# Optimization experiments

Measured on AMD Instinct MI355X. Metric: run time of the kernel, lower is better.

The kernel has to match this reference:

```python
import jax, jax.numpy as jnp
import numpy as np

# irreps multiplicities: node = NSx0e + NVx1o, edge = ESx0e + EVx1o, hidden = HSx0e + HVx1o
NS, NV = 64, 32
ES, EV = 8, 8
HS, HV = 96, 32          # Gate splits HS scalars -> (HS-HV) silu scalars + HV sigmoid gates
N_NODES, N_EDGES = 10000, 100000
INV_SQRT3 = float(1.0 / np.sqrt(3.0))  # w3j(1,1,0) coefficient


def _split(x, ns, nv):
    # [N, ns + 3*nv] -> scalars [N, ns], vectors [N, nv, 3]
    return x[:, :ns], x[:, ns:].reshape(x.shape[0], nv, 3)


def _merge(s, v):
    return jnp.concatenate([s, v.reshape(v.shape[0], -1)], axis=-1)


def _fc_tp(xs, xv, ys, yv, w_ss, w_vv, w_sv, w_vs):
    """FullyConnectedTensorProduct for l<=1 irreps with path ('element') normalization.
    Paths: 0e*0e->0e, 1o*1o->0e (dot/sqrt3), 0e*1o->1o, 1o*0e->1o."""
    fan_s = w_ss.shape[0] * w_ss.shape[1] + w_vv.shape[0] * w_vv.shape[1]
    fan_v = w_sv.shape[0] * w_sv.shape[1] + w_vs.shape[0] * w_vs.shape[1]
    out_s = (jnp.einsum('eu,ev,uvw->ew', xs, ys, w_ss)
             + INV_SQRT3 * jnp.einsum('eum,evm,uvw->ew', xv, yv, w_vv)) / np.sqrt(fan_s)
    out_v = (jnp.einsum('eu,evm,uvw->ewm', xs, yv, w_sv)
             + jnp.einsum('eum,ev,uvw->ewm', xv, ys, w_vs)) / np.sqrt(fan_v)
    return out_s, out_v


def _gate(s, v, n_plain):
    # e3nn Gate: silu on plain scalars, sigmoid gates multiply each vector channel
    plain = jax.nn.silu(s[:, :n_plain])
    gates = jax.nn.sigmoid(s[:, n_plain:])
    return plain, v * gates[:, :, None]


def _lin(s, v, Ws, Wv):
    # e3nn equivariant Linear: mixes multiplicities per irrep, shared over m, 1/sqrt(fan_in)
    return (s @ Ws) / np.sqrt(Ws.shape[0]), jnp.einsum('num,uw->nwm', v, Wv) / np.sqrt(Wv.shape[0])


def setup_inputs() -> dict:
    key = jax.random.key(0)
    ks = jax.random.split(key, 15)
    rn = lambda k, sh: jax.random.normal(k, sh, dtype=jnp.float32)
    return {
        'node_features': rn(ks[0], (N_NODES, NS + 3 * NV)),
        'edge_attr': rn(ks[1], (N_EDGES, ES + 3 * EV)),
        'w_msg_ss': rn(ks[2], (NS, ES, HS)),
        'w_msg_vv': rn(ks[3], (NV, EV, HS)),
        'w_msg_sv': rn(ks[4], (NS, EV, HV)),
        'w_msg_vs': rn(ks[5], (NV, ES, HV)),
        'w_lin_msg_s': rn(ks[6], (HS - HV, HS)),
        'w_lin_msg_v': rn(ks[7], (HV, HV)),
        'w_upd_ss': rn(ks[8], (NS, HS, HS)),
        'w_upd_vv': rn(ks[9], (NV, HV, HS)),
        'w_upd_sv': rn(ks[10], (NS, HV, HV)),
        'w_upd_vs': rn(ks[11], (NV, HS, HV)),
        'w_lin_upd_s': rn(ks[12], (HS - HV, NS)),
        'w_lin_upd_v': rn(ks[13], (HV, NV)),
        'edge_index': jax.random.randint(ks[14], (2, N_EDGES), 0, N_NODES),
    }


def reference(node_features, edge_attr, w_msg_ss, w_msg_vv, w_msg_sv, w_msg_vs,
              w_lin_msg_s, w_lin_msg_v, w_upd_ss, w_upd_vv, w_upd_sv, w_upd_vs,
              w_lin_upd_s, w_lin_upd_v, edge_index):
    row, col = edge_index[0], edge_index[1]
    ns, nv = _split(node_features, NS, NV)
    es, ev = _split(edge_attr, ES, EV)

    # messages: gather -> CG tensor product -> gate -> linear
    ms, mv = _fc_tp(ns[col], nv[col], es, ev, w_msg_ss, w_msg_vv, w_msg_sv, w_msg_vs)
    ps, pv = _gate(ms, mv, HS - HV)                  # [E, HS-HV], [E, HV, 3]
    ls, lv = _lin(ps, pv, w_lin_msg_s, w_lin_msg_v)  # [E, HS],    [E, HV, 3]

    # scatter-sum aggregation onto destination nodes
    agg_s = jax.ops.segment_sum(ls, row, num_segments=N_NODES)
    agg_v = jax.ops.segment_sum(lv, row, num_segments=N_NODES)

    # node update: CG tensor product with aggregated messages -> gate -> linear -> residual
    us, uv = _fc_tp(ns, nv, agg_s, agg_v, w_upd_ss, w_upd_vv, w_upd_sv, w_upd_vs)
    gs, gv = _gate(us, uv, HS - HV)
    ds, dv = _lin(gs, gv, w_lin_upd_s, w_lin_upd_v)  # [N, NS], [N, NV, 3]
    return _merge(ns + ds, nv + dv)
```

## Files before the change

kernel.cpp:

```cpp
#include <hip/hip_runtime.h>
#include <hip/hip_bf16.h>

constexpr int kNodes = 10000;
constexpr int kEdges = 100000;

constexpr float INV_SQRT3    = 0.57735026918962576f;
constexpr float INV_SQRT768  = 0.036084391824351615f;
constexpr float INV_SQRT7168 = 0.011811389781538352f;
constexpr float INV_SQRT5120 = 0.013975424859373686f;
constexpr float INV_SQRT32   = 0.17677669529663687f;

constexpr size_t MSGW_OFF  = 0;
constexpr size_t UPDW1_OFF = 245760;
constexpr size_t UPDW2_OFF = 2080768;
constexpr size_t MLIN_OFF  = 2572288;
constexpr size_t ULIN_OFF  = 2588672;

typedef __attribute__((ext_vector_type(8))) short bf8;
typedef __attribute__((ext_vector_type(4))) float f4;
union BF { bf8 v; short s[8]; unsigned u[4]; };

__device__ __forceinline__ short f2bf(float f) {
    union { float f; unsigned u; } c; c.f = f;
    unsigned r = c.u + 0x7fffu + ((c.u >> 16) & 1u);
    return (short)(r >> 16);
}
__device__ __forceinline__ unsigned pk2(float lo, float hi) {
    union { __hip_bfloat162 h; unsigned u; } c;
    c.h = __float22bfloat162_rn(make_float2(lo, hi));
    return c.u;
}
__device__ __forceinline__ f4 mfma16(bf8 a, bf8 b, f4 c) {
    return __builtin_amdgcn_mfma_f32_16x16x32_bf16(a, b, c, 0, 0, 0);
}
__device__ __forceinline__ void gl2lds(const void* g, void* l) {
    __builtin_amdgcn_global_load_lds(
        (const __attribute__((address_space(1))) unsigned int*)g,
        (__attribute__((address_space(3))) unsigned int*)l, 16, 0, 0);
}
__device__ __forceinline__ float fsig(float x) { return 1.0f / (1.0f + __expf(-x)); }

__global__ void prep_kernel(
    const float* __restrict__ Wmss, const float* __restrict__ Wmvv,
    const float* __restrict__ Wmsv, const float* __restrict__ Wmvs,
    const float* __restrict__ Wlms, const float* __restrict__ Wlmv,
    const float* __restrict__ Wuss, const float* __restrict__ Wuvv,
    const float* __restrict__ Wusv, const float* __restrict__ Wuvs,
    const float* __restrict__ Wlus, const float* __restrict__ Wluv,
    char* __restrict__ wout)
{
    int i = blockIdx.x * 256 + threadIdx.x;
    float v = 0.f;
    short* dst;
    if (i < 122880) {
        dst = (short*)(wout + MSGW_OFF) + i;
        int t = i / 5120, q = i % 5120, r = q / 40, c = q % 40;
        if (c < 32) {
            int k = t * 32 + c;
            if (r < 96) {
                v = (k < 512 ? Wmss[k * 96 + r]
                             : Wmvv[(k - 512) * 96 + r] * INV_SQRT3) * INV_SQRT768;
            } else {
                int n2 = r - 96;
                if (k < 512) { int u = k & 63, vv = k >> 6; v = Wmsv[(u * 8 + vv) * 32 + n2] * INV_SQRT768; }
                else         { v = Wmvs[(k - 512) * 32 + n2] * INV_SQRT768; }
            }
        }
    } else if (i < 1040384) {
        int j = i - 122880;
        dst = (short*)(wout + UPDW1_OFF) + j;
        int t = j / 4096, q = j % 4096, r = q / 40, c = q % 40;
        if (q < 3840 && c < 32) {
            int k = t * 32 + c;
            if (k < 6144) { int u = k & 63, vv = k >> 6;
                v = Wuss[(u * 96 + vv) * 96 + r] * INV_SQRT7168; }
            else { int r2 = k - 6144; int u = r2 & 31, vv = r2 >> 5;
                v = Wuvv[(u * 32 + vv) * 96 + r] * (INV_SQRT3 * INV_SQRT7168); }
        }
    } else if (i < 1286144) {
        int j = i - 1040384;
        dst = (short*)(wout + UPDW2_OFF) + j;
        int t = j / 1536, q = j % 1536, r = q / 40, c = q % 40;
        if (q < 1280 && c < 32) {
            int k = t * 32 + c;
            if (k < 2048) { int u = k & 63, vv = k >> 6;
                v = Wusv[(u * 32 + vv) * 32 + r] * INV_SQRT5120; }
            else { int r2 = k - 2048;
                v = Wuvs[r2 * 32 + r] * INV_SQRT5120; }
        }
    } else if (i < 1294336) {
        int j = i - 1286144;
        dst = (short*)(wout + MLIN_OFF) + j;
        if (j < 6912) { int n = j / 72, kk = j % 72; if (kk < 64) v = Wlms[kk * 96 + n] * 0.125f; }
        else { int j2 = j - 6912; int n = j2 / 40, kk = j2 % 40; if (kk < 32) v = Wlmv[kk * 32 + n] * INV_SQRT32; }
    } else if (i < 1300480) {
        int j = i - 1294336;
        dst = (short*)(wout + ULIN_OFF) + j;
        if (j < 4608) { int n = j / 72, kk = j % 72; if (kk < 64) v = Wlus[kk * 64 + n] * 0.125f; }
        else if (j < 5888) { int j2 = j - 4608; int n = j2 / 40, kk = j2 % 40; if (kk < 32) v = Wluv[kk * 32 + n] * INV_SQRT32; }
        else v = 0.f;
    } else return;
    *dst = f2bf(v);
}

__global__ __launch_bounds__(256, 2) void msg_kernel(
    const float* __restrict__ nf, const float* __restrict__ ea,
    const int* __restrict__ eidx, const char* __restrict__ wout,
    float* __restrict__ agg)
{
    __shared__ char pool[79488];
    float* nf_sh  = (float*)pool;
    float* ea_sh  = (float*)(pool + 20992);
    int*   row_sh = (int*)  (pool + 25600);
    short* wbuf   = (short*)(pool + 25728);
    short* lin    = (short*)(pool + 46208);
    float* gat    = (float*)(pool + 62592);
    short* silu_s = (short*)(pool + 67200);
    short* pv_s   = (short*)(pool + 71808);

    const int t = threadIdx.x, w = t >> 6, lane = t & 63;
    const int l15 = lane & 15, lg = lane >> 4;
    const int eblk = blockIdx.x * 32;

    const char* msgW = wout + MSGW_OFF;
    const char* mlin = wout + MLIN_OFF;

    for (int c = w; c < 16; c += 4) gl2lds(mlin + c * 1024 + lane * 16, (char*)lin + c * 1024);
    for (int c = w; c < 10; c += 4) gl2lds(msgW + c * 1024 + lane * 16, (char*)wbuf + c * 1024);

    {
        const int i = t >> 3, j = t & 7;
        const int e = eblk + i;
        if (j == 0) row_sh[i] = eidx[e];
        const int col = eidx[kEdges + e];
        const float4* src = (const float4*)(nf + (size_t)col * 160);
        for (int c = j; c < 40; c += 8) *(float4*)&nf_sh[i * 164 + c * 4] = src[c];
        const float4* esrc = (const float4*)(ea + (size_t)e * 32);
        *(float4*)&ea_sh[i * 36 + j * 4] = esrc[j];
    }
    __syncthreads();

    f4 accS[3] = {{0.f,0.f,0.f,0.f},{0.f,0.f,0.f,0.f},{0.f,0.f,0.f,0.f}};
    f4 accV[3] = {{0.f,0.f,0.f,0.f},{0.f,0.f,0.f,0.f},{0.f,0.f,0.f,0.f}};
    const int Ms = w >> 1, nb = (w & 1) * 3;
    const int es_ = Ms * 16 + l15;

    const float4 ey0 = *(const float4*)&ea_sh[es_ * 36];
    const float4 ey1 = *(const float4*)&ea_sh[es_ * 36 + 4];
    float eyv[24];
    #pragma unroll
    for (int q = 0; q < 6; ++q)
        *(float4*)&eyv[q * 4] = *(const float4*)&ea_sh[es_ * 36 + 8 + q * 4];

    for (int kt = 0; kt < 24; ++kt) {
        const short* wb = wbuf + (kt & 1) * 5120;
        if (kt + 1 < 24)
            for (int c = w; c < 10; c += 4)
                gl2lds(msgW + (kt + 1) * 10240 + c * 1024 + lane * 16,
                       (char*)(wbuf + ((kt + 1) & 1) * 5120) + c * 1024);

        BF aS;
        if (kt < 16) {
            const int uu = kt * 4 + lg;
            const float xs = nf_sh[es_ * 164 + uu];
            aS.u[0] = pk2(xs * ey0.x, xs * ey0.y);
            aS.u[1] = pk2(xs * ey0.z, xs * ey0.w);
            aS.u[2] = pk2(xs * ey1.x, xs * ey1.y);
            aS.u[3] = pk2(xs * ey1.z, xs * ey1.w);
        } else {
            const int uu = (kt - 16) * 4 + lg;
            const float* xp = &nf_sh[es_ * 164 + 64 + 3 * uu];
            const float x0 = xp[0], x1 = xp[1], x2 = xp[2];
            #pragma unroll
            for (int j = 0; j < 4; ++j) {
                float a0 = x0 * eyv[6*j  ] + x1 * eyv[6*j+1] + x2 * eyv[6*j+2];
                float a1 = x0 * eyv[6*j+3] + x1 * eyv[6*j+4] + x2 * eyv[6*j+5];
                aS.u[j] = pk2(a0, a1);
            }
        }
        #pragma unroll
        for (int i = 0; i < 3; ++i) {
            bf8 b = *(const bf8*)&wb[((nb + i) * 16 + l15) * 40 + lg * 8];
            accS[i] = mfma16(aS.v, b, accS[i]);
        }

        BF aV; int prevMv = -1;
        #pragma unroll
        for (int i = 0; i < 3; ++i) {
            const int tv = 3 * w + i, Mv = tv >> 1, Nv = tv & 1;
            if (Mv != prevMv) {
                prevMv = Mv;
                const int m = Mv >> 1, ev = (Mv & 1) * 16 + l15;
                if (kt < 16) {
                    const int kp = kt * 32 + lg * 8;
                    const int vv = kp >> 6, u0 = kp & 63;
                    const float ym = ea_sh[ev * 36 + 8 + 3 * vv + m];
                    const float4 x0 = *(const float4*)&nf_sh[ev * 164 + u0];
                    const float4 x1 = *(const float4*)&nf_sh[ev * 164 + u0 + 4];
                    aV.u[0] = pk2(x0.x * ym, x0.y * ym);
                    aV.u[1] = pk2(x0.z * ym, x0.w * ym);
                    aV.u[2] = pk2(x1.x * ym, x1.y * ym);
                    aV.u[3] = pk2(x1.z * ym, x1.w * ym);
                } else {
                    const int uu = (kt - 16) * 4 + lg;
                    const float xm = nf_sh[ev * 164 + 64 + 3 * uu + m];
                    const float4 y0 = *(const float4*)&ea_sh[ev * 36];
                    const float4 y1 = *(const float4*)&ea_sh[ev * 36 + 4];
                    aV.u[0] = pk2(xm * y0.x, xm * y0.y);
                    aV.u[1] = pk2(xm * y0.z, xm * y0.w);
                    aV.u[2] = pk2(xm * y1.x, xm * y1.y);
                    aV.u[3] = pk2(xm * y1.z, xm * y1.w);
                }
            }
            bf8 b = *(const bf8*)&wb[3840 + (Nv * 16 + l15) * 40 + lg * 8];
            accV[i] = mfma16(aV.v, b, accV[i]);
        }
        __syncthreads();
    }

    #pragma unroll
    for (int i = 0; i < 3; ++i) {
        const int n = (nb + i) * 16 + l15;
        #pragma unroll
        for (int r = 0; r < 4; ++r) {
            const int e = Ms * 16 + lg * 4 + r;
            const float v = accS[i][r];
            if (n < 64) silu_s[e * 72 + n] = f2bf(v * fsig(v));
            else        gat[e * 36 + (n - 64)] = fsig(v);
        }
    }
    __syncthreads();
    #pragma unroll
    for (int i = 0; i < 3; ++i) {
        const int tv = 3 * w + i, Mv = tv >> 1, Nv = tv & 1;
        const int m = Mv >> 1, eb = (Mv & 1) * 16;
        const int u = Nv * 16 + l15;
        #pragma unroll
        for (int r = 0; r < 4; ++r) {
            const int e = eb + lg * 4 + r;
            pv_s[(m * 32 + e) * 40 + u] = f2bf(accV[i][r] * gat[e * 36 + u]);
        }
    }
    __syncthreads();

    {
        f4 acc[3] = {{0.f,0.f,0.f,0.f},{0.f,0.f,0.f,0.f},{0.f,0.f,0.f,0.f}};
        #pragma unroll
        for (int k0 = 0; k0 < 2; ++k0) {
            const int kg = k0 * 32 + lg * 8;
            bf8 a = *(const bf8*)&silu_s[es_ * 72 + kg];
            #pragma unroll
            for (int i = 0; i < 3; ++i) {
                bf8 b = *(const bf8*)&lin[((nb + i) * 16 + l15) * 72 + kg];
                acc[i] = mfma16(a, b, acc[i]);
            }
        }
        #pragma unroll
        for (int i = 0; i < 3; ++i) {
            const int n = (nb + i) * 16 + l15;
            #pragma unroll
            for (int r = 0; r < 4; ++r) {
                const int e = Ms * 16 + lg * 4 + r;
                atomicAdd(&agg[(size_t)row_sh[e] * 192 + n], acc[i][r]);
            }
        }
    }
    {
        f4 acc[3] = {{0.f,0.f,0.f,0.f},{0.f,0.f,0.f,0.f},{0.f,0.f,0.f,0.f}};
        const int kg = lg * 8;
        BF a; int prevMv = -1;
        #pragma unroll
        for (int i = 0; i < 3; ++i) {
            const int tv = 3 * w + i, Mv = tv >> 1, Nv = tv & 1;
            if (Mv != prevMv) { prevMv = Mv; a.v = *(const bf8*)&pv_s[(Mv * 16 + l15) * 40 + kg]; }
            bf8 b = *(const bf8*)&lin[6912 + (Nv * 16 + l15) * 40 + kg];
            acc[i] = mfma16(a.v, b, acc[i]);
        }
        #pragma unroll
        for (int i = 0; i < 3; ++i) {
            const int tv = 3 * w + i, Mv = tv >> 1, Nv = tv & 1;
            const int w2 = Nv * 16 + l15;
            #pragma unroll
            for (int r = 0; r < 4; ++r) {
                const int rr = Mv * 16 + lg * 4 + r;
                const int m = rr >> 5, e = rr & 31;
                atomicAdd(&agg[(size_t)row_sh[e] * 192 + 96 + w2 * 3 + m], acc[i][r]);
            }
        }
    }
}

__global__ __launch_bounds__(512, 1) void upd_kernel(
    const float* __restrict__ nf, const char* __restrict__ wout,
    float* __restrict__ agg)
{
    __shared__ char pool[140800];
    float* nf_sh  = (float*)pool;
    float* ag_sh  = (float*)(pool + 20992);
    short* wbuf   = (short*)(pool + 46080);
    short* lin    = (short*)(pool + 111616);
    float* gat    = (float*)(pool + 123904);
    short* silu_s = (short*)(pool + 128512);
    short* gv_s   = (short*)(pool + 133120);
    float* red    = (float*)(pool + 46080);

    const int t = threadIdx.x, w = t >> 6, lane = t & 63;
    const int g = w >> 2, wl = w & 3;
    const int l15 = lane & 15, lg = lane >> 4;
    const int nblk = blockIdx.x * 32;
    const char* W1 = wout + UPDW1_OFF;
    const char* W2 = wout + UPDW2_OFF;
    short* const gw = wbuf + g * 16384;

    for (int c = w; c < 12; c += 8) gl2lds(wout + ULIN_OFF + c * 1024 + lane * 16, (char*)lin + c * 1024);
    for (int c = wl; c < 16; c += 4)
        gl2lds(W1 + (size_t)g * 112 * 8192 + c * 1024 + lane * 16, (char*)gw + c * 1024);

    {
        const int i = t >> 4, j = t & 15;
        int n = nblk + i; if (n > kNodes - 1) n = kNodes - 1;
        const float4* src = (const float4*)(nf + (size_t)n * 160);
        for (int c = j; c < 40; c += 16) *(float4*)&nf_sh[i * 164 + c * 4] = src[c];
        const float4* asrc = (const float4*)(agg + (size_t)n * 192);
        for (int c = j; c < 48; c += 16) *(float4*)&ag_sh[i * 196 + c * 4] = asrc[c];
    }
    __syncthreads();

    const int Ms = wl >> 1, nb = (wl & 1) * 3;
    const int es_ = Ms * 16 + l15;

    f4 accS[3] = {{0.f,0.f,0.f,0.f},{0.f,0.f,0.f,0.f},{0.f,0.f,0.f,0.f}};
    for (int s = 0; s < 56; ++s) {
        if (s + 1 < 56)
            for (int c = wl; c < 16; c += 4)
                gl2lds(W1 + (size_t)(g * 112 + (s + 1) * 2) * 8192 + c * 1024 + lane * 16,
                       (char*)(gw + ((s + 1) & 1) * 8192) + c * 1024);
        #pragma unroll
        for (int tl = 0; tl < 2; ++tl) {
            const int kt = g * 112 + s * 2 + tl;
            const short* wb = gw + (s & 1) * 8192 + tl * 4096;
            BF aS;
            if (kt < 192) {
                const int kp = kt * 32 + lg * 8;
                const int vv = kp >> 6, u0 = kp & 63;
                const float ys = ag_sh[es_ * 196 + vv];
                const float4 x0 = *(const float4*)&nf_sh[es_ * 164 + u0];
                const float4 x1 = *(const float4*)&nf_sh[es_ * 164 + u0 + 4];
                aS.u[0] = pk2(x0.x * ys, x0.y * ys);
                aS.u[1] = pk2(x0.z * ys, x0.w * ys);
                aS.u[2] = pk2(x1.x * ys, x1.y * ys);
                aS.u[3] = pk2(x1.z * ys, x1.w * ys);
            } else {
                const int rp = kt * 32 + lg * 8 - 6144;
                const int vv = rp >> 5, u0 = rp & 31;
                const float* xp = &nf_sh[es_ * 164 + 64 + 3 * u0];
                const float* gp = &ag_sh[es_ * 196 + 96 + 3 * vv];
                const float g0 = gp[0], g1 = gp[1], g2 = gp[2];
                #pragma unroll
                for (int j = 0; j < 4; ++j) {
                    float a0 = xp[6*j  ] * g0 + xp[6*j+1] * g1 + xp[6*j+2] * g2;
                    float a1 = xp[6*j+3] * g0 + xp[6*j+4] * g1 + xp[6*j+5] * g2;
                    aS.u[j] = pk2(a0, a1);
                }
            }
            #pragma unroll
            for (int i = 0; i < 3; ++i) {
                bf8 b = *(const bf8*)&wb[((nb + i) * 16 + l15) * 40 + lg * 8];
                accS[i] = mfma16(aS.v, b, accS[i]);
            }
        }
        __syncthreads();
    }

    if (g == 1) {
        #pragma unroll
        for (int i = 0; i < 3; ++i) {
            const int n = (nb + i) * 16 + l15;
            #pragma unroll
            for (int r = 0; r < 4; ++r)
                red[(Ms * 16 + lg * 4 + r) * 96 + n] = accS[i][r];
        }
    }
    __syncthreads();
    if (g == 0) {
        #pragma unroll
        for (int i = 0; i < 3; ++i) {
            const int n = (nb + i) * 16 + l15;
            #pragma unroll
            for (int r = 0; r < 4; ++r) {
                const int e = Ms * 16 + lg * 4 + r;
                const float v = accS[i][r] + red[e * 96 + n];
                if (n < 64) silu_s[e * 72 + n] = f2bf(v * fsig(v));
                else        gat[e * 36 + (n - 64)] = fsig(v);
            }
        }
    }
    __syncthreads();
    for (int c = wl; c < 12; c += 4)
        gl2lds(W2 + (size_t)g * 80 * 3072 + c * 1024 + lane * 16, (char*)gw + c * 1024);
    __syncthreads();

    f4 accV[3] = {{0.f,0.f,0.f,0.f},{0.f,0.f,0.f,0.f},{0.f,0.f,0.f,0.f}};
    for (int s = 0; s < 20; ++s) {
        if (s + 1 < 20)
            for (int c = wl; c < 12; c += 4)
                gl2lds(W2 + (size_t)(g * 80 + (s + 1) * 4) * 3072 + c * 1024 + lane * 16,
                       (char*)(gw + ((s + 1) & 1) * 6144) + c * 1024);
        #pragma unroll
        for (int tl = 0; tl < 4; ++tl) {
            const int kt = g * 80 + s * 4 + tl;
            const short* wb = gw + (s & 1) * 6144 + tl * 1536;
            BF aV; int prevMv = -1;
            #pragma unroll
            for (int i = 0; i < 3; ++i) {
                const int tv = 3 * wl + i, Mv = tv >> 1, Nv = tv & 1;
                if (Mv != prevMv) {
                    prevMv = Mv;
                    const int m = Mv >> 1, ev = (Mv & 1) * 16 + l15;
                    if (kt < 64) {
                        const int kp = kt * 32 + lg * 8;
                        const int vv = kp >> 6, u0 = kp & 63;
                        const float ym = ag_sh[ev * 196 + 96 + 3 * vv + m];
                        const float4 x0 = *(const float4*)&nf_sh[ev * 164 + u0];
                        const float4 x1 = *(const float4*)&nf_sh[ev * 164 + u0 + 4];
                        aV.u[0] = pk2(x0.x * ym, x0.y * ym);
                        aV.u[1] = pk2(x0.z * ym, x0.w * ym);
                        aV.u[2] = pk2(x1.x * ym, x1.y * ym);
                        aV.u[3] = pk2(x1.z * ym, x1.w * ym);
                    } else {
                        const int rp = kt * 32 + lg * 8 - 2048;
                        const int u = rp / 96, v0 = rp - u * 96;
                        const float xm = nf_sh[ev * 164 + 64 + 3 * u + m];
                        const float4 y0 = *(const float4*)&ag_sh[ev * 196 + v0];
                        const float4 y1 = *(const float4*)&ag_sh[ev * 196 + v0 + 4];
                        aV.u[0] = pk2(xm * y0.x, xm * y0.y);
                        aV.u[1] = pk2(xm * y0.z, xm * y0.w);
                        aV.u[2] = pk2(xm * y1.x, xm * y1.y);
                        aV.u[3] = pk2(xm * y1.z, xm * y1.w);
                    }
                }
                bf8 b = *(const bf8*)&wb[(Nv * 16 + l15) * 40 + lg * 8];
                accV[i] = mfma16(aV.v, b, accV[i]);
            }
        }
        __syncthreads();
    }

    if (g == 1) {
        #pragma unroll
        for (int i = 0; i < 3; ++i) {
            const int tv = 3 * wl + i, Mv = tv >> 1, Nv = tv & 1;
            #pragma unroll
            for (int r = 0; r < 4; ++r)
                red[(Mv * 16 + lg * 4 + r) * 32 + Nv * 16 + l15] = accV[i][r];
        }
    }
    __syncthreads();
    if (g == 0) {
        #pragma unroll
        for (int i = 0; i < 3; ++i) {
            const int tv = 3 * wl + i, Mv = tv >> 1, Nv = tv & 1;
            const int m = Mv >> 1, eb = (Mv & 1) * 16;
            const int u = Nv * 16 + l15;
            #pragma unroll
            for (int r = 0; r < 4; ++r) {
                const int e = eb + lg * 4 + r;
                const float v = accV[i][r] + red[(Mv * 16 + lg * 4 + r) * 32 + u];
                gv_s[(m * 32 + e) * 40 + u] = f2bf(v * gat[e * 36 + u]);
            }
        }
    }
    __syncthreads();

    const int nvalid = kNodes - nblk;
    if (g == 0) {
        {
            f4 acc[2] = {{0.f,0.f,0.f,0.f},{0.f,0.f,0.f,0.f}};
            const int nb2 = (wl & 1) * 2;
            #pragma unroll
            for (int k0 = 0; k0 < 2; ++k0) {
                const int kg = k0 * 32 + lg * 8;
                bf8 a = *(const bf8*)&silu_s[es_ * 72 + kg];
                #pragma unroll
                for (int i = 0; i < 2; ++i) {
                    bf8 b = *(const bf8*)&lin[((nb2 + i) * 16 + l15) * 72 + kg];
                    acc[i] = mfma16(a, b, acc[i]);
                }
            }
            #pragma unroll
            for (int i = 0; i < 2; ++i) {
                const int n = (nb2 + i) * 16 + l15;
                #pragma unroll
                for (int r = 0; r < 4; ++r) {
                    const int e = Ms * 16 + lg * 4 + r;
                    if (e < nvalid)
                        agg[(size_t)(nblk + e) * 192 + n] = nf_sh[e * 164 + n] + acc[i][r];
                }
            }
        }
        {
            f4 acc[3] = {{0.f,0.f,0.f,0.f},{0.f,0.f,0.f,0.f},{0.f,0.f,0.f,0.f}};
            const int kg = lg * 8;
            BF a; int prevMv = -1;
            #pragma unroll
            for (int i = 0; i < 3; ++i) {
                const int tv = 3 * wl + i, Mv = tv >> 1, Nv = tv & 1;
                if (Mv != prevMv) { prevMv = Mv; a.v = *(const bf8*)&gv_s[(Mv * 16 + l15) * 40 + kg]; }
                bf8 b = *(const bf8*)&lin[4608 + (Nv * 16 + l15) * 40 + kg];
                acc[i] = mfma16(a.v, b, acc[i]);
            }
            #pragma unroll
            for (int i = 0; i < 3; ++i) {
                const int tv = 3 * wl + i, Mv = tv >> 1, Nv = tv & 1;
                const int w2 = Nv * 16 + l15;
                #pragma unroll
                for (int r = 0; r < 4; ++r) {
                    const int rr = Mv * 16 + lg * 4 + r;
                    const int m = rr >> 5, e = rr & 31;
                    if (e < nvalid)
                        agg[(size_t)(nblk + e) * 192 + 64 + w2 * 3 + m]
                            = nf_sh[e * 164 + 64 + w2 * 3 + m] + acc[i][r];
                }
            }
        }
    }
}

__global__ __launch_bounds__(256) void copy_kernel(const float* __restrict__ agg,
                                                   float* __restrict__ out)
{
    int i = blockIdx.x * 256 + threadIdx.x;
    if (i < 400000) {
        int n = i / 40, c = i - n * 40;
        ((float4*)out)[i] = ((const float4*)agg)[n * 48 + c];
    }
}

extern "C" void kernel_launch(void* const* d_in, const int* in_sizes, int n_in,
                              void* d_out, int out_size, void* d_ws, size_t ws_size,
                              hipStream_t stream) {
    const float* nf   = (const float*)d_in[0];
    const float* ea   = (const float*)d_in[1];
    const int*   eidx = (const int*)d_in[14];
    float* agg = (float*)d_ws;
    char*  wout = (char*)d_out;

    hipMemsetAsync(agg, 0, 7680000, stream);
    prep_kernel<<<5080, 256, 0, stream>>>(
        (const float*)d_in[2], (const float*)d_in[3], (const float*)d_in[4],
        (const float*)d_in[5], (const float*)d_in[6], (const float*)d_in[7],
        (const float*)d_in[8], (const float*)d_in[9], (const float*)d_in[10],
        (const float*)d_in[11], (const float*)d_in[12], (const float*)d_in[13], wout);
    msg_kernel<<<kEdges / 32, 256, 0, stream>>>(nf, ea, eidx, wout, agg);
    upd_kernel<<<(kNodes + 31) / 32, 512, 0, stream>>>(nf, wout, agg);
    copy_kernel<<<1563, 256, 0, stream>>>(agg, (float*)d_out);
}
```

Measured before the change: 524.3 us.

## Read MFMA weight fragments directly from global memory instead of LDS staging

Removes the double-buffered global-to-LDS weight staging (and its per-iteration barriers) in the message and update kernels, reading bf16 weight B-fragments straight from global/L2 with a packed unpadded layout. The smaller LDS footprint lets occupancy rise (launch bounds raised to 3 and 4 blocks per CU). It risks higher global load latency in the MFMA inner loops and duplicated L2 traffic across waves, and it changes the prepared weight layout and prep kernel size.

```diff
diff --git a/kernel.cpp b/kernel.cpp
--- a/kernel.cpp
+++ b/kernel.cpp
@@ -11,10 +11,12 @@
 constexpr float INV_SQRT32   = 0.17677669529663687f;
 
 constexpr size_t MSGW_OFF  = 0;
-constexpr size_t UPDW1_OFF = 245760;
-constexpr size_t UPDW2_OFF = 2080768;
-constexpr size_t MLIN_OFF  = 2572288;
-constexpr size_t ULIN_OFF  = 2588672;
+constexpr size_t UPDW1_OFF = 196608;
+constexpr size_t UPDW2_OFF = 1572864;
+constexpr size_t MLINS_OFF = 1900544;
+constexpr size_t MLINV_OFF = 1912832;
+constexpr size_t ULINS_OFF = 1914880;
+constexpr size_t ULINV_OFF = 1923072;
 
 typedef __attribute__((ext_vector_type(8))) short bf8;
 typedef __attribute__((ext_vector_type(4))) float f4;
@@ -33,10 +35,8 @@
 __device__ __forceinline__ f4 mfma16(bf8 a, bf8 b, f4 c) {
     return __builtin_amdgcn_mfma_f32_16x16x32_bf16(a, b, c, 0, 0, 0);
 }
-__device__ __forceinline__ void gl2lds(const void* g, void* l) {
-    __builtin_amdgcn_global_load_lds(
-        (const __attribute__((address_space(1))) unsigned int*)g,
-        (__attribute__((address_space(3))) unsigned int*)l, 16, 0, 0);
+__device__ __forceinline__ bf8 ldB(const char* p) {
+    return *(const bf8*)p;
 }
 __device__ __forceinline__ float fsig(float x) { return 1.0f / (1.0f + __expf(-x)); }
 
@@ -50,83 +50,79 @@
     char* __restrict__ wout)
 {
     int i = blockIdx.x * 256 + threadIdx.x;
-    float v = 0.f;
+    float v;
     short* dst;
-    if (i < 122880) {
+    if (i < 98304) {
         dst = (short*)(wout + MSGW_OFF) + i;
-        int t = i / 5120, q = i % 5120, r = q / 40, c = q % 40;
-        if (c < 32) {
-            int k = t * 32 + c;
-            if (r < 96) {
-                v = (k < 512 ? Wmss[k * 96 + r]
-                             : Wmvv[(k - 512) * 96 + r] * INV_SQRT3) * INV_SQRT768;
-            } else {
-                int n2 = r - 96;
-                if (k < 512) { int u = k & 63, vv = k >> 6; v = Wmsv[(u * 8 + vv) * 32 + n2] * INV_SQRT768; }
-                else         { v = Wmvs[(k - 512) * 32 + n2] * INV_SQRT768; }
-            }
-        }
-    } else if (i < 1040384) {
-        int j = i - 122880;
+        int t = i >> 12, q = i & 4095, r = q >> 5, c = q & 31;
+        int k = t * 32 + c;
+        if (r < 96) {
+            v = (k < 512 ? Wmss[k * 96 + r]
+                         : Wmvv[(k - 512) * 96 + r] * INV_SQRT3) * INV_SQRT768;
+        } else {
+            int n2 = r - 96;
+            if (k < 512) { int u = k & 63, vv = k >> 6; v = Wmsv[(u * 8 + vv) * 32 + n2] * INV_SQRT768; }
+            else         { v = Wmvs[(k - 512) * 32 + n2] * INV_SQRT768; }
+        }
+    } else if (i < 786432) {
+        int j = i - 98304;
         dst = (short*)(wout + UPDW1_OFF) + j;
-        int t = j / 4096, q = j % 4096, r = q / 40, c = q % 40;
-        if (q < 3840 && c < 32) {
-            int k = t * 32 + c;
-            if (k < 6144) { int u = k & 63, vv = k >> 6;
-                v = Wuss[(u * 96 + vv) * 96 + r] * INV_SQRT7168; }
-            else { int r2 = k - 6144; int u = r2 & 31, vv = r2 >> 5;
-                v = Wuvv[(u * 32 + vv) * 96 + r] * (INV_SQRT3 * INV_SQRT7168); }
-        }
-    } else if (i < 1286144) {
-        int j = i - 1040384;
+        int t = j / 3072, q = j % 3072, r = q >> 5, c = q & 31;
+        int k = t * 32 + c;
+        if (k < 6144) { int u = k & 63, vv = k >> 6;
+            v = Wuss[(u * 96 + vv) * 96 + r] * INV_SQRT7168; }
+        else { int r2 = k - 6144; int u = r2 & 31, vv = r2 >> 5;
+            v = Wuvv[(u * 32 + vv) * 96 + r] * (INV_SQRT3 * INV_SQRT7168); }
+    } else if (i < 950272) {
+        int j = i - 786432;
         dst = (short*)(wout + UPDW2_OFF) + j;
-        int t = j / 1536, q = j % 1536, r = q / 40, c = q % 40;
-        if (q < 1280 && c < 32) {
-            int k = t * 32 + c;
-            if (k < 2048) { int u = k & 63, vv = k >> 6;
-                v = Wusv[(u * 32 + vv) * 32 + r] * INV_SQRT5120; }
-            else { int r2 = k - 2048;
-                v = Wuvs[r2 * 32 + r] * INV_SQRT5120; }
-        }
-    } else if (i < 1294336) {
-        int j = i - 1286144;
-        dst = (short*)(wout + MLIN_OFF) + j;
-        if (j < 6912) { int n = j / 72, kk = j % 72; if (kk < 64) v = Wlms[kk * 96 + n] * 0.125f; }
-        else { int j2 = j - 6912; int n = j2 / 40, kk = j2 % 40; if (kk < 32) v = Wlmv[kk * 32 + n] * INV_SQRT32; }
-    } else if (i < 1300480) {
-        int j = i - 1294336;
-        dst = (short*)(wout + ULIN_OFF) + j;
-        if (j < 4608) { int n = j / 72, kk = j % 72; if (kk < 64) v = Wlus[kk * 64 + n] * 0.125f; }
-        else if (j < 5888) { int j2 = j - 4608; int n = j2 / 40, kk = j2 % 40; if (kk < 32) v = Wluv[kk * 32 + n] * INV_SQRT32; }
-        else v = 0.f;
+        int t = j >> 10, q = j & 1023, r = q >> 5, c = q & 31;
+        int k = t * 32 + c;
+        if (k < 2048) { int u = k & 63, vv = k >> 6;
+            v = Wusv[(u * 32 + vv) * 32 + r] * INV_SQRT5120; }
+        else { int r2 = k - 2048;
+            v = Wuvs[r2 * 32 + r] * INV_SQRT5120; }
+    } else if (i < 956416) {
+        int j = i - 950272;
+        dst = (short*)(wout + MLINS_OFF) + j;
+        int n = j >> 6, kk = j & 63;
+        v = Wlms[kk * 96 + n] * 0.125f;
+    } else if (i < 957440) {
+        int j = i - 956416;
+        dst = (short*)(wout + MLINV_OFF) + j;
+        int n = j >> 5, kk = j & 31;
+        v = Wlmv[kk * 32 + n] * INV_SQRT32;
+    } else if (i < 961536) {
+        int j = i - 957440;
+        dst = (short*)(wout + ULINS_OFF) + j;
+        int n = j >> 6, kk = j & 63;
+        v = Wlus[kk * 64 + n] * 0.125f;
+    } else if (i < 962560) {
+        int j = i - 961536;
+        dst = (short*)(wout + ULINV_OFF) + j;
+        int n = j >> 5, kk = j & 31;
+        v = Wluv[kk * 32 + n] * INV_SQRT32;
     } else return;
     *dst = f2bf(v);
 }
 
-__global__ __launch_bounds__(256, 2) void msg_kernel(
+__global__ __launch_bounds__(256, 3) void msg_kernel(
     const float* __restrict__ nf, const float* __restrict__ ea,
     const int* __restrict__ eidx, const char* __restrict__ wout,
     float* __restrict__ agg)
 {
-    __shared__ char pool[79488];
-    float* nf_sh  = (float*)pool;
-    float* ea_sh  = (float*)(pool + 20992);
-    int*   row_sh = (int*)  (pool + 25600);
-    short* wbuf   = (short*)(pool + 25728);
-    short* lin    = (short*)(pool + 46208);
-    float* gat    = (float*)(pool + 62592);
-    short* silu_s = (short*)(pool + 67200);
-    short* pv_s   = (short*)(pool + 71808);
+    __shared__ float nf_sh[32 * 164];
+    __shared__ float ea_sh[32 * 36];
+    __shared__ int   row_sh[32];
+    __shared__ float gat[32 * 36];
+    __shared__ short silu_s[32 * 72];
+    __shared__ short pv_s[96 * 40];
 
     const int t = threadIdx.x, w = t >> 6, lane = t & 63;
     const int l15 = lane & 15, lg = lane >> 4;
     const int eblk = blockIdx.x * 32;
 
     const char* msgW = wout + MSGW_OFF;
-    const char* mlin = wout + MLIN_OFF;
-
-    for (int c = w; c < 16; c += 4) gl2lds(mlin + c * 1024 + lane * 16, (char*)lin + c * 1024);
-    for (int c = w; c < 10; c += 4) gl2lds(msgW + c * 1024 + lane * 16, (char*)wbuf + c * 1024);
 
     {
         const int i = t >> 3, j = t & 7;
@@ -152,22 +148,45 @@
     for (int q = 0; q < 6; ++q)
         *(float4*)&eyv[q * 4] = *(const float4*)&ea_sh[es_ * 36 + 8 + q * 4];
 
-    for (int kt = 0; kt < 24; ++kt) {
-        const short* wb = wbuf + (kt & 1) * 5120;
-        if (kt + 1 < 24)
-            for (int c = w; c < 10; c += 4)
-                gl2lds(msgW + (kt + 1) * 10240 + c * 1024 + lane * 16,
-                       (char*)(wbuf + ((kt + 1) & 1) * 5120) + c * 1024);
-
+    for (int kt = 0; kt < 16; ++kt) {
+        const char* wb = msgW + kt * 8192;
         BF aS;
-        if (kt < 16) {
+        {
             const int uu = kt * 4 + lg;
             const float xs = nf_sh[es_ * 164 + uu];
             aS.u[0] = pk2(xs * ey0.x, xs * ey0.y);
             aS.u[1] = pk2(xs * ey0.z, xs * ey0.w);
             aS.u[2] = pk2(xs * ey1.x, xs * ey1.y);
             aS.u[3] = pk2(xs * ey1.z, xs * ey1.w);
-        } else {
+        }
+        #pragma unroll
+        for (int i = 0; i < 3; ++i)
+            accS[i] = mfma16(aS.v, ldB(wb + ((nb + i) * 16 + l15) * 64 + lg * 16), accS[i]);
+
+        BF aV; int prevMv = -1;
+        #pragma unroll
+        for (int i = 0; i < 3; ++i) {
+            const int tv = 3 * w + i, Mv = tv >> 1, Nv = tv & 1;
+            if (Mv != prevMv) {
+                prevMv = Mv;
+                const int m = Mv >> 1, ev = (Mv & 1) * 16 + l15;
+                const int kp = kt * 32 + lg * 8;
+                const int vv = kp >> 6, u0 = kp & 63;
+                const float ym = ea_sh[ev * 36 + 8 + 3 * vv + m];
+                const float4 x0 = *(const float4*)&nf_sh[ev * 164 + u0];
+                const float4 x1 = *(const float4*)&nf_sh[ev * 164 + u0 + 4];
+                aV.u[0] = pk2(x0.x * ym, x0.y * ym);
+                aV.u[1] = pk2(x0.z * ym, x0.w * ym);
+                aV.u[2] = pk2(x1.x * ym, x1.y * ym);
+                aV.u[3] = pk2(x1.z * ym, x1.w * ym);
+            }
+            accV[i] = mfma16(aV.v, ldB(wb + (96 + (Nv * 16 + l15)) * 64 + lg * 16), accV[i]);
+        }
+    }
+    for (int kt = 16; kt < 24; ++kt) {
+        const char* wb = msgW + kt * 8192;
+        BF aS;
+        {
             const int uu = (kt - 16) * 4 + lg;
             const float* xp = &nf_sh[es_ * 164 + 64 + 3 * uu];
             const float x0 = xp[0], x1 = xp[1], x2 = xp[2];
@@ -179,10 +198,8 @@
             }
         }
         #pragma unroll
-        for (int i = 0; i < 3; ++i) {
-            bf8 b = *(const bf8*)&wb[((nb + i) * 16 + l15) * 40 + lg * 8];
-            accS[i] = mfma16(aS.v, b, accS[i]);
-        }
+        for (int i = 0; i < 3; ++i)
+            accS[i] = mfma16(aS.v, ldB(wb + ((nb + i) * 16 + l15) * 64 + lg * 16), accS[i]);
 
         BF aV; int prevMv = -1;
         #pragma unroll
@@ -191,31 +208,17 @@
             if (Mv != prevMv) {
                 prevMv = Mv;
                 const int m = Mv >> 1, ev = (Mv & 1) * 16 + l15;
-                if (kt < 16) {
-                    const int kp = kt * 32 + lg * 8;
-                    const int vv = kp >> 6, u0 = kp & 63;
-                    const float ym = ea_sh[ev * 36 + 8 + 3 * vv + m];
-                    const float4 x0 = *(const float4*)&nf_sh[ev * 164 + u0];
-                    const float4 x1 = *(const float4*)&nf_sh[ev * 164 + u0 + 4];
-                    aV.u[0] = pk2(x0.x * ym, x0.y * ym);
-                    aV.u[1] = pk2(x0.z * ym, x0.w * ym);
-                    aV.u[2] = pk2(x1.x * ym, x1.y * ym);
-                    aV.u[3] = pk2(x1.z * ym, x1.w * ym);
-                } else {
-                    const int uu = (kt - 16) * 4 + lg;
-                    const float xm = nf_sh[ev * 164 + 64 + 3 * uu + m];
-                    const float4 y0 = *(const float4*)&ea_sh[ev * 36];
-                    const float4 y1 = *(const float4*)&ea_sh[ev * 36 + 4];
-                    aV.u[0] = pk2(xm * y0.x, xm * y0.y);
-                    aV.u[1] = pk2(xm * y0.z, xm * y0.w);
-                    aV.u[2] = pk2(xm * y1.x, xm * y1.y);
-                    aV.u[3] = pk2(xm * y1.z, xm * y1.w);
-                }
-            }
-            bf8 b = *(const bf8*)&wb[3840 + (Nv * 16 + l15) * 40 + lg * 8];
-            accV[i] = mfma16(aV.v, b, accV[i]);
-        }
-        __syncthreads();
+                const int uu = (kt - 16) * 4 + lg;
+                const float xm = nf_sh[ev * 164 + 64 + 3 * uu + m];
+                const float4 y0 = *(const float4*)&ea_sh[ev * 36];
+                const float4 y1 = *(const float4*)&ea_sh[ev * 36 + 4];
+                aV.u[0] = pk2(xm * y0.x, xm * y0.y);
+                aV.u[1] = pk2(xm * y0.z, xm * y0.w);
+                aV.u[2] = pk2(xm * y1.x, xm * y1.y);
+                aV.u[3] = pk2(xm * y1.z, xm * y1.w);
+            }
+            accV[i] = mfma16(aV.v, ldB(wb + (96 + (Nv * 16 + l15)) * 64 + lg * 16), accV[i]);
+        }
     }
 
     #pragma unroll
@@ -244,16 +247,15 @@
     __syncthreads();
 
     {
+        const char* mls = wout + MLINS_OFF;
         f4 acc[3] = {{0.f,0.f,0.f,0.f},{0.f,0.f,0.f,0.f},{0.f,0.f,0.f,0.f}};
         #pragma unroll
         for (int k0 = 0; k0 < 2; ++k0) {
             const int kg = k0 * 32 + lg * 8;
             bf8 a = *(const bf8*)&silu_s[es_ * 72 + kg];
             #pragma unroll
-            for (int i = 0; i < 3; ++i) {
-                bf8 b = *(const bf8*)&lin[((nb + i) * 16 + l15) * 72 + kg];
-                acc[i] = mfma16(a, b, acc[i]);
-            }
+            for (int i = 0; i < 3; ++i)
+                acc[i] = mfma16(a, ldB(mls + ((nb + i) * 16 + l15) * 128 + kg * 2), acc[i]);
         }
         #pragma unroll
         for (int i = 0; i < 3; ++i) {
@@ -266,6 +268,7 @@
         }
     }
     {
+        const char* mlv = wout + MLINV_OFF;
         f4 acc[3] = {{0.f,0.f,0.f,0.f},{0.f,0.f,0.f,0.f},{0.f,0.f,0.f,0.f}};
         const int kg = lg * 8;
         BF a; int prevMv = -1;
@@ -273,8 +276,7 @@
         for (int i = 0; i < 3; ++i) {
             const int tv = 3 * w + i, Mv = tv >> 1, Nv = tv & 1;
             if (Mv != prevMv) { prevMv = Mv; a.v = *(const bf8*)&pv_s[(Mv * 16 + l15) * 40 + kg]; }
-            bf8 b = *(const bf8*)&lin[6912 + (Nv * 16 + l15) * 40 + kg];
-            acc[i] = mfma16(a.v, b, acc[i]);
+            acc[i] = mfma16(a.v, ldB(mlv + (Nv * 16 + l15) * 64 + kg * 2), acc[i]);
         }
         #pragma unroll
         for (int i = 0; i < 3; ++i) {
@@ -290,19 +292,16 @@
     }
 }
 
-__global__ __launch_bounds__(512, 1) void upd_kernel(
+__global__ __launch_bounds__(512, 4) void upd_kernel(
     const float* __restrict__ nf, const char* __restrict__ wout,
     float* __restrict__ agg)
 {
-    __shared__ char pool[140800];
-    float* nf_sh  = (float*)pool;
-    float* ag_sh  = (float*)(pool + 20992);
-    short* wbuf   = (short*)(pool + 46080);
-    short* lin    = (short*)(pool + 111616);
-    float* gat    = (float*)(pool + 123904);
-    short* silu_s = (short*)(pool + 128512);
-    short* gv_s   = (short*)(pool + 133120);
-    float* red    = (float*)(pool + 46080);
+    __shared__ float nf_sh[32 * 164];
+    __shared__ float ag_sh[32 * 196];
+    __shared__ float gat[32 * 36];
+    __shared__ short silu_s[32 * 72];
+    __shared__ short gv_s[96 * 40];
+    __shared__ float red[3072];
 
     const int t = threadIdx.x, w = t >> 6, lane = t & 63;
     const int g = w >> 2, wl = w & 3;
@@ -310,11 +309,6 @@
     const int nblk = blockIdx.x * 32;
     const char* W1 = wout + UPDW1_OFF;
     const char* W2 = wout + UPDW2_OFF;
-    short* const gw = wbuf + g * 16384;
-
-    for (int c = w; c < 12; c += 8) gl2lds(wout + ULIN_OFF + c * 1024 + lane * 16, (char*)lin + c * 1024);
-    for (int c = wl; c < 16; c += 4)
-        gl2lds(W1 + (size_t)g * 112 * 8192 + c * 1024 + lane * 16, (char*)gw + c * 1024);
 
     {
         const int i = t >> 4, j = t & 15;
@@ -330,46 +324,44 @@
     const int es_ = Ms * 16 + l15;
 
     f4 accS[3] = {{0.f,0.f,0.f,0.f},{0.f,0.f,0.f,0.f},{0.f,0.f,0.f,0.f}};
-    for (int s = 0; s < 56; ++s) {
-        if (s + 1 < 56)
-            for (int c = wl; c < 16; c += 4)
-                gl2lds(W1 + (size_t)(g * 112 + (s + 1) * 2) * 8192 + c * 1024 + lane * 16,
-                       (char*)(gw + ((s + 1) & 1) * 8192) + c * 1024);
-        #pragma unroll
-        for (int tl = 0; tl < 2; ++tl) {
-            const int kt = g * 112 + s * 2 + tl;
-            const short* wb = gw + (s & 1) * 8192 + tl * 4096;
+    {
+        const int kt0 = g * 112, kt1 = kt0 + 112;
+        const int ktSS = kt1 < 192 ? kt1 : 192;
+        int kt = kt0;
+        for (; kt < ktSS; ++kt) {
+            const char* wb = W1 + (size_t)kt * 6144;
+            const int kp = kt * 32 + lg * 8;
+            const int vv = kp >> 6, u0 = kp & 63;
+            const float ys = ag_sh[es_ * 196 + vv];
+            const float4 x0 = *(const float4*)&nf_sh[es_ * 164 + u0];
+            const float4 x1 = *(const float4*)&nf_sh[es_ * 164 + u0 + 4];
             BF aS;
-            if (kt < 192) {
-                const int kp = kt * 32 + lg * 8;
-                const int vv = kp >> 6, u0 = kp & 63;
-                const float ys = ag_sh[es_ * 196 + vv];
-                const float4 x0 = *(const float4*)&nf_sh[es_ * 164 + u0];
-                const float4 x1 = *(const float4*)&nf_sh[es_ * 164 + u0 + 4];
-                aS.u[0] = pk2(x0.x * ys, x0.y * ys);
-                aS.u[1] = pk2(x0.z * ys, x0.w * ys);
-                aS.u[2] = pk2(x1.x * ys, x1.y * ys);
-                aS.u[3] = pk2(x1.z * ys, x1.w * ys);
-            } else {
-                const int rp = kt * 32 + lg * 8 - 6144;
-                const int vv = rp >> 5, u0 = rp & 31;
-                const float* xp = &nf_sh[es_ * 164 + 64 + 3 * u0];
-                const float* gp = &ag_sh[es_ * 196 + 96 + 3 * vv];
-                const float g0 = gp[0], g1 = gp[1], g2 = gp[2];
-                #pragma unroll
-                for (int j = 0; j < 4; ++j) {
-                    float a0 = xp[6*j  ] * g0 + xp[6*j+1] * g1 + xp[6*j+2] * g2;
-                    float a1 = xp[6*j+3] * g0 + xp[6*j+4] * g1 + xp[6*j+5] * g2;
-                    aS.u[j] = pk2(a0, a1);
-                }
-            }
-            #pragma unroll
-            for (int i = 0; i < 3; ++i) {
-                bf8 b = *(const bf8*)&wb[((nb + i) * 16 + l15) * 40 + lg * 8];
-                accS[i] = mfma16(aS.v, b, accS[i]);
-            }
-        }
-        __syncthreads();
+            aS.u[0] = pk2(x0.x * ys, x0.y * ys);
+            aS.u[1] = pk2(x0.z * ys, x0.w * ys);
+            aS.u[2] = pk2(x1.x * ys, x1.y * ys);
+            aS.u[3] = pk2(x1.z * ys, x1.w * ys);
+            #pragma unroll
+            for (int i = 0; i < 3; ++i)
+                accS[i] = mfma16(aS.v, ldB(wb + ((nb + i) * 16 + l15) * 64 + lg * 16), accS[i]);
+        }
+        for (; kt < kt1; ++kt) {
+            const char* wb = W1 + (size_t)kt * 6144;
+            const int rp = kt * 32 + lg * 8 - 6144;
+            const int vv = rp >> 5, u0 = rp & 31;
+            const float* xp = &nf_sh[es_ * 164 + 64 + 3 * u0];
+            const float* gp = &ag_sh[es_ * 196 + 96 + 3 * vv];
+            const float g0 = gp[0], g1 = gp[1], g2 = gp[2];
+            BF aS;
+            #pragma unroll
+            for (int j = 0; j < 4; ++j) {
+                float a0 = xp[6*j  ] * g0 + xp[6*j+1] * g1 + xp[6*j+2] * g2;
+                float a1 = xp[6*j+3] * g0 + xp[6*j+4] * g1 + xp[6*j+5] * g2;
+                aS.u[j] = pk2(a0, a1);
+            }
+            #pragma unroll
+            for (int i = 0; i < 3; ++i)
+                accS[i] = mfma16(aS.v, ldB(wb + ((nb + i) * 16 + l15) * 64 + lg * 16), accS[i]);
+        }
     }
 
     if (g == 1) {
@@ -396,20 +388,14 @@
         }
     }
     __syncthreads();
-    for (int c = wl; c < 12; c += 4)
-        gl2lds(W2 + (size_t)g * 80 * 3072 + c * 1024 + lane * 16, (char*)gw + c * 1024);
-    __syncthreads();
 
     f4 accV[3] = {{0.f,0.f,0.f,0.f},{0.f,0.f,0.f,0.f},{0.f,0.f,0.f,0.f}};
-    for (int s = 0; s < 20; ++s) {
-        if (s + 1 < 20)
-            for (int c = wl; c < 12; c += 4)
-                gl2lds(W2 + (size_t)(g * 80 + (s + 1) * 4) * 3072 + c * 1024 + lane * 16,
-                       (char*)(gw + ((s + 1) & 1) * 6144) + c * 1024);
-        #pragma unroll
-        for (int tl = 0; tl < 4; ++tl) {
-            const int kt = g * 80 + s * 4 + tl;
-            const short* wb = gw + (s & 1) * 6144 + tl * 1536;
+    {
+        const int kt0 = g * 80, kt1 = kt0 + 80;
+        const int ktSV = kt1 < 64 ? kt1 : 64;
+        int kt = kt0;
+        for (; kt < ktSV; ++kt) {
+            const char* wb = W2 + (size_t)kt * 2048;
             BF aV; int prevMv = -1;
             #pragma unroll
             for (int i = 0; i < 3; ++i) {
@@ -417,33 +403,41 @@
                 if (Mv != prevMv) {
                     prevMv = Mv;
                     const int m = Mv >> 1, ev = (Mv & 1) * 16 + l15;
-                    if (kt < 64) {
-                        const int kp = kt * 32 + lg * 8;
-                        const int vv = kp >> 6, u0 = kp & 63;
-                        const float ym = ag_sh[ev * 196 + 96 + 3 * vv + m];
-                        const float4 x0 = *(const float4*)&nf_sh[ev * 164 + u0];
-                        const float4 x1 = *(const float4*)&nf_sh[ev * 164 + u0 + 4];
-                        aV.u[0] = pk2(x0.x * ym, x0.y * ym);
-                        aV.u[1] = pk2(x0.z * ym, x0.w * ym);
-                        aV.u[2] = pk2(x1.x * ym, x1.y * ym);
-                        aV.u[3] = pk2(x1.z * ym, x1.w * ym);
-                    } else {
-                        const int rp = kt * 32 + lg * 8 - 2048;
-                        const int u = rp / 96, v0 = rp - u * 96;
-                        const float xm = nf_sh[ev * 164 + 64 + 3 * u + m];
-                        const float4 y0 = *(const float4*)&ag_sh[ev * 196 + v0];
-                        const float4 y1 = *(const float4*)&ag_sh[ev * 196 + v0 + 4];
-                        aV.u[0] = pk2(xm * y0.x, xm * y0.y);
-                        aV.u[1] = pk2(xm * y0.z, xm * y0.w);
-                        aV.u[2] = pk2(xm * y1.x, xm * y1.y);
-                        aV.u[3] = pk2(xm * y1.z, xm * y1.w);
-                    }
+                    const int kp = kt * 32 + lg * 8;
+                    const int vv = kp >> 6, u0 = kp & 63;
+                    const float ym = ag_sh[ev * 196 + 96 + 3 * vv + m];
+                    const float4 x0 = *(const float4*)&nf_sh[ev * 164 + u0];
+                    const float4 x1 = *(const float4*)&nf_sh[ev * 164 + u0 + 4];
+                    aV.u[0] = pk2(x0.x * ym, x0.y * ym);
+                    aV.u[1] = pk2(x0.z * ym, x0.w * ym);
+                    aV.u[2] = pk2(x1.x * ym, x1.y * ym);
+                    aV.u[3] = pk2(x1.z * ym, x1.w * ym);
                 }
-                bf8 b = *(const bf8*)&wb[(Nv * 16 + l15) * 40 + lg * 8];
-                accV[i] = mfma16(aV.v, b, accV[i]);
-            }
-        }
-        __syncthreads();
+                accV[i] = mfma16(aV.v, ldB(wb + (Nv * 16 + l15) * 64 + lg * 16), accV[i]);
+            }
+        }
+        for (; kt < kt1; ++kt) {
+            const char* wb = W2 + (size_t)kt * 2048;
+            BF aV; int prevMv = -1;
+            #pragma unroll
+            for (int i = 0; i < 3; ++i) {
+                const int tv = 3 * wl + i, Mv = tv >> 1, Nv = tv & 1;
+                if (Mv != prevMv) {
+                    prevMv = Mv;
+                    const int m = Mv >> 1, ev = (Mv & 1) * 16 + l15;
+                    const int rp = kt * 32 + lg * 8 - 2048;
+                    const int u = rp / 96, v0 = rp - u * 96;
+                    const float xm = nf_sh[ev * 164 + 64 + 3 * u + m];
+                    const float4 y0 = *(const float4*)&ag_sh[ev * 196 + v0];
+                    const float4 y1 = *(const float4*)&ag_sh[ev * 196 + v0 + 4];
+                    aV.u[0] = pk2(xm * y0.x, xm * y0.y);
+                    aV.u[1] = pk2(xm * y0.z, xm * y0.w);
+                    aV.u[2] = pk2(xm * y1.x, xm * y1.y);
+                    aV.u[3] = pk2(xm * y1.z, xm * y1.w);
+                }
+                accV[i] = mfma16(aV.v, ldB(wb + (Nv * 16 + l15) * 64 + lg * 16), accV[i]);
+            }
+        }
     }
 
     if (g == 1) {
@@ -475,6 +469,7 @@
     const int nvalid = kNodes - nblk;
     if (g == 0) {
         {
+            const char* uls = wout + ULINS_OFF;
             f4 acc[2] = {{0.f,0.f,0.f,0.f},{0.f,0.f,0.f,0.f}};
             const int nb2 = (wl & 1) * 2;
             #pragma unroll
@@ -482,10 +477,8 @@
                 const int kg = k0 * 32 + lg * 8;
                 bf8 a = *(const bf8*)&silu_s[es_ * 72 + kg];
                 #pragma unroll
-                for (int i = 0; i < 2; ++i) {
-                    bf8 b = *(const bf8*)&lin[((nb2 + i) * 16 + l15) * 72 + kg];
-                    acc[i] = mfma16(a, b, acc[i]);
-                }
+                for (int i = 0; i < 2; ++i)
+                    acc[i] = mfma16(a, ldB(uls + ((nb2 + i) * 16 + l15) * 128 + kg * 2), acc[i]);
             }
             #pragma unroll
             for (int i = 0; i < 2; ++i) {
@@ -499,6 +492,7 @@
             }
         }
         {
+            const char* ulv = wout + ULINV_OFF;
             f4 acc[3] = {{0.f,0.f,0.f,0.f},{0.f,0.f,0.f,0.f},{0.f,0.f,0.f,0.f}};
             const int kg = lg * 8;
             BF a; int prevMv = -1;
@@ -506,8 +500,7 @@
             for (int i = 0; i < 3; ++i) {
                 const int tv = 3 * wl + i, Mv = tv >> 1, Nv = tv & 1;
                 if (Mv != prevMv) { prevMv = Mv; a.v = *(const bf8*)&gv_s[(Mv * 16 + l15) * 40 + kg]; }
-                bf8 b = *(const bf8*)&lin[4608 + (Nv * 16 + l15) * 40 + kg];
-                acc[i] = mfma16(a.v, b, acc[i]);
+                acc[i] = mfma16(a.v, ldB(ulv + (Nv * 16 + l15) * 64 + kg * 2), acc[i]);
             }
             #pragma unroll
             for (int i = 0; i < 3; ++i) {
@@ -546,7 +539,7 @@
     char*  wout = (char*)d_out;
 
     hipMemsetAsync(agg, 0, 7680000, stream);
-    prep_kernel<<<5080, 256, 0, stream>>>(
+    prep_kernel<<<3760, 256, 0, stream>>>(
         (const float*)d_in[2], (const float*)d_in[3], (const float*)d_in[4],
         (const float*)d_in[5], (const float*)d_in[6], (const float*)d_in[7],
         (const float*)d_in[8], (const float*)d_in[9], (const float*)d_in[10],
```

Measured after the change: 463.3 us. -11.6%, faster.
